# Optimization experiments

Measured on AMD Instinct MI355X. Metric: run time of the kernel, lower is better.

Reference implementation:

```python
import jax, jax.numpy as jnp
import numpy as np

N_HEAD = 8
NORM_GROUPS = 32
EPS = 1e-6


def setup_inputs() -> dict:
    key = jax.random.key(0)
    ks = jax.random.split(key, 9)
    B, C, H, W, D = 1, 256, 16, 16, 16
    COND = 512
    x = jax.random.normal(ks[0], (B, C, H, W, D), dtype=jnp.float32)
    cond = jax.random.normal(ks[1], (B, COND), dtype=jnp.float32)
    # AdaGN linear scale/shift (torch Linear: weight [C, cond_dim], bias [C])
    w_scale = jax.random.normal(ks[2], (C, COND), dtype=jnp.float32) * 0.02
    b_scale = jax.random.normal(ks[3], (C,), dtype=jnp.float32) * 0.02
    w_shift = jax.random.normal(ks[4], (C, COND), dtype=jnp.float32) * 0.02
    b_shift = jax.random.normal(ks[5], (C,), dtype=jnp.float32) * 0.02
    # 1x1x1 conv3d weights collapse to matrices: qkv [3C, C] (no bias), out [C, C] + bias
    w_qkv = jax.random.normal(ks[6], (3 * C, C), dtype=jnp.float32) * (1.0 / np.sqrt(C))
    w_out = jax.random.normal(ks[7], (C, C), dtype=jnp.float32) * (1.0 / np.sqrt(C))
    b_out = jax.random.normal(ks[8], (C,), dtype=jnp.float32) * 0.02
    return {"x": x, "cond": cond, "w_scale": w_scale, "b_scale": b_scale,
            "w_shift": w_shift, "b_shift": b_shift, "w_qkv": w_qkv,
            "w_out": w_out, "b_out": b_out}


def _ada_gn(x, cond, w_scale, b_scale, w_shift, b_shift):
    B, C, H, W, D = x.shape
    G = NORM_GROUPS
    xg = x.reshape(B, G, C // G, H, W, D)
    mean = jnp.mean(xg, axis=(2, 3, 4, 5), keepdims=True)
    var = jnp.var(xg, axis=(2, 3, 4, 5), keepdims=True)
    x_norm = ((xg - mean) * jax.lax.rsqrt(var + EPS)).reshape(B, C, H, W, D)
    scale = (cond @ w_scale.T + b_scale)[:, :, None, None, None]  # [B,C,1,1,1]
    shift = (cond @ w_shift.T + b_shift)[:, :, None, None, None]
    return x_norm * (1.0 + scale) + shift


def reference(x, cond, w_scale, b_scale, w_shift, b_shift, w_qkv, w_out, b_out):
    B, C, H, W, D = x.shape
    nh = N_HEAD
    hd = C // nh
    N = H * W * D  # flattened spatial tokens
    norm = _ada_gn(x, cond, w_scale, b_scale, w_shift, b_shift)
    # 1x1x1 conv == channel matmul
    qkv = jnp.einsum('oc,bchwd->bohwd', w_qkv, norm)        # [B,3C,H,W,D]
    qkv = qkv.reshape(B, nh, 3 * hd, N)
    q, k, v = jnp.split(qkv, 3, axis=2)                      # each [B,nh,hd,N]
    attn = jnp.einsum('bnci,bncj->bnij', q, k) / jnp.sqrt(jnp.float32(C))
    attn = jax.nn.softmax(attn, axis=-1)                     # [B,nh,N,N]
    out = jnp.einsum('bnij,bncj->bnci', attn, v)             # [B,nh,hd,N]
    out = out.reshape(B, C, H, W, D)
    out = jnp.einsum('oc,bchwd->bohwd', w_out, out) + b_out[None, :, None, None, None]
    return out + x
```

## Files before the change

kernel.cpp:

```cpp
#include <hip/hip_runtime.h>
#include <math.h>

#define CCH 256
#define NN  4096
#define NHEAD 8
#define CONDD 512

typedef __attribute__((ext_vector_type(8))) short short8;
typedef __attribute__((ext_vector_type(4))) float f32x4;
typedef __attribute__((ext_vector_type(16))) float f32x16;

static __device__ __forceinline__ short f2bf(float f) {
    union { float f; uint32_t u; } v; v.f = f;
    uint32_t r = v.u + 0x7fffu + ((v.u >> 16) & 1u);
    return (short)(r >> 16);
}

static __device__ __forceinline__ uint32_t cvt_pk_bf16(float a, float b) {
    uint32_t r;
    asm("v_cvt_pk_bf16_f32 %0, %1, %2" : "=v"(r) : "v"(a), "v"(b));
    return r;
}

__global__ __launch_bounds__(256) void front_fused(const float* __restrict__ x,
                                                   const float* __restrict__ cond,
                                                   const float* __restrict__ w_scale,
                                                   const float* __restrict__ b_scale,
                                                   const float* __restrict__ w_shift,
                                                   const float* __restrict__ b_shift,
                                                   const float* __restrict__ wq,
                                                   const float* __restrict__ wo,
                                                   float* __restrict__ partial,
                                                   float* __restrict__ scale,
                                                   float* __restrict__ shift,
                                                   short* __restrict__ wqb,
                                                   short* __restrict__ wob) {
    __shared__ float rs[4], rss[4];
    int bb = blockIdx.x;
    int t = threadIdx.x;
    if (bb < 256) {
        const float4* p = (const float4*)(x + bb * 4096);
        float s = 0.f, ss = 0.f;
        for (int k = t; k < 1024; k += 256) {
            float4 v = p[k];
            s += v.x + v.y + v.z + v.w;
            ss += v.x * v.x + v.y * v.y + v.z * v.z + v.w * v.w;
        }
        #pragma unroll
        for (int off = 32; off; off >>= 1) { s += __shfl_xor(s, off); ss += __shfl_xor(ss, off); }
        int wid = t >> 6;
        if ((t & 63) == 0) { rs[wid] = s; rss[wid] = ss; }
        __syncthreads();
        if (t == 0) {
            partial[2 * bb] = rs[0] + rs[1] + rs[2] + rs[3];
            partial[2 * bb + 1] = rss[0] + rss[1] + rss[2] + rss[3];
        }
    } else if (bb < 1280) {
        int idx = (bb - 256) * 256 + t;
        if (idx < 196608) wqb[idx] = f2bf(wq[idx]);
        else              wob[idx - 196608] = f2bf(wo[idx - 196608]);
    } else {
        int o = (bb - 1280) * 4 + (t >> 6);
        int lane = t & 63;
        float ds = 0.f, dh = 0.f;
        for (int k = lane; k < CONDD; k += 64) {
            float cv = cond[k];
            ds += cv * w_scale[o * CONDD + k];
            dh += cv * w_shift[o * CONDD + k];
        }
        #pragma unroll
        for (int off = 32; off; off >>= 1) { ds += __shfl_xor(ds, off); dh += __shfl_xor(dh, off); }
        if (lane == 0) { scale[o] = ds + b_scale[o]; shift[o] = dh + b_shift[o]; }
    }
}

__global__ __launch_bounds__(256) void normalize_t(const float* __restrict__ x,
                                                   const float* __restrict__ partial,
                                                   const float* __restrict__ scale,
                                                   const float* __restrict__ shift,
                                                   short* __restrict__ norm_t) {
    __shared__ float gm[8], gr[8];
    __shared__ float Aa[64], Bb[64];
    __shared__ short tile[32 * 66];
    int i0 = blockIdx.x * 32;
    int c0 = blockIdx.y * 64;
    int g0 = c0 >> 3;
    int t = threadIdx.x;
    if (t < 8) {
        float s = 0.f, ss = 0.f;
        #pragma unroll
        for (int ch = 0; ch < 8; ++ch) {
            s += partial[((g0 + t) * 8 + ch) * 2];
            ss += partial[((g0 + t) * 8 + ch) * 2 + 1];
        }
        float mean = s * (1.0f / 32768.0f);
        float var = ss * (1.0f / 32768.0f) - mean * mean;
        gm[t] = mean;
        gr[t] = rsqrtf(var + 1e-6f);
    }
    __syncthreads();
    if (t < 64) {
        int c = c0 + t;
        float a = gr[t >> 3] * (1.0f + scale[c]);
        Aa[t] = a;
        Bb[t] = shift[c] - gm[t >> 3] * a;
    }
    __syncthreads();
    #pragma unroll
    for (int e0 = 0; e0 < 8; ++e0) {
        int e = e0 * 256 + t;
        int cl = e >> 5, il = e & 31;
        float v = x[(c0 + cl) * NN + i0 + il];
        tile[il * 66 + cl] = f2bf(v * Aa[cl] + Bb[cl]);
    }
    __syncthreads();
    #pragma unroll
    for (int e0 = 0; e0 < 4; ++e0) {
        int e = e0 * 256 + t;
        int il = e >> 5, cd = e & 31;
        uint32_t d = *(const uint32_t*)&tile[il * 66 + 2 * cd];
        *(uint32_t*)&norm_t[(i0 + il) * 256 + c0 + 2 * cd] = d;
    }
}

__global__ __launch_bounds__(256) void qkv_gemm(const short* __restrict__ wqb,
                                                const short* __restrict__ norm_t,
                                                short* __restrict__ qtb, short* __restrict__ ktb,
                                                short* __restrict__ vcb) {
    int t = threadIdx.x;
    int w = t >> 6, lane = t & 63, li = lane & 15, lg = lane >> 4;
    int o0 = blockIdx.x * 32;
    int i0 = blockIdx.y * 64 + w * 16;
    f32x4 acc[2] = {{0,0,0,0},{0,0,0,0}};
    const short* bbase = norm_t + (i0 + li) * 256 + 8 * lg;
    const short* abase = wqb + (o0 + li) * 256 + 8 * lg;
    #pragma unroll
    for (int ks = 0; ks < 8; ++ks) {
        short8 bfrag = *(const short8*)(bbase + ks * 32);
        #pragma unroll
        for (int f = 0; f < 2; ++f) {
            short8 afrag = *(const short8*)(abase + f * 16 * 256 + ks * 32);
            acc[f] = __builtin_amdgcn_mfma_f32_16x16x32_bf16(afrag, bfrag, acc[f], 0, 0, 0);
        }
    }
    int i = i0 + li;
    #pragma unroll
    for (int f = 0; f < 2; ++f) {
        #pragma unroll
        for (int r = 0; r < 4; ++r) {
            int o = o0 + 16 * f + 4 * lg + r;
            float v = acc[f][r];
            int h = o / 96;
            int rr = o - h * 96;
            int cc = rr & 31;
            int kind = rr >> 5;
            if (kind == 0)      qtb[(h * NN + i) * 32 + cc] = f2bf(v * (0.0625f * 1.44269504f));
            else if (kind == 1) ktb[(h * NN + i) * 32 + cc] = f2bf(v);
            else                vcb[(h * 32 + cc) * NN + i] = f2bf(v);
        }
    }
}

__global__ __launch_bounds__(256, 4) void attention_mfma(const short* __restrict__ qtb,
                                                         const short* __restrict__ ktb,
                                                         const short* __restrict__ vcb,
                                                         short* __restrict__ attnT) {
    __shared__ float lds_acc[4][32][32];
    __shared__ float lds_lsum[4][32];

    int bid = blockIdx.x;
    int h = bid & 7;
    int i_base = (bid >> 3) * 32;
    int t = threadIdx.x;
    int w = t >> 6, lane = t & 63, l31 = lane & 31, hi = lane >> 5;

    const short* qrow = qtb + (h * NN + i_base + l31) * 32;
    short8 qf0 = *(const short8*)(qrow + 8 * hi);
    short8 qf1 = *(const short8*)(qrow + 16 + 8 * hi);

    const short* kbase = ktb + (h * NN + l31) * 32 + 8 * hi;
    const short* vrow  = vcb + (h * 32 + l31) * NN + 8 * hi;

    f32x16 acc = {0,0,0,0,0,0,0,0,0,0,0,0,0,0,0,0};
    const f32x16 zero16 = {0,0,0,0,0,0,0,0,0,0,0,0,0,0,0,0};
    float lsum = 0.f;

    int jstart = w * 1024;
    int jend = jstart + 1024;

    short8 kf0 = *(const short8*)(kbase + jstart * 32);
    short8 kf1 = *(const short8*)(kbase + jstart * 32 + 16);
    short8 kf2 = *(const short8*)(kbase + (jstart + 32) * 32);
    short8 kf3 = *(const short8*)(kbase + (jstart + 32) * 32 + 16);

    #pragma unroll 1
    for (int j = jstart; j < jend; j += 64) {
        short8 vf0 = *(const short8*)(vrow + j);
        short8 vf1 = *(const short8*)(vrow + j + 16);
        short8 vf2 = *(const short8*)(vrow + j + 32);
        short8 vf3 = *(const short8*)(vrow + j + 48);

        __builtin_amdgcn_s_setprio(1);
        f32x16 sa = __builtin_amdgcn_mfma_f32_32x32x16_bf16(kf0, qf0, zero16, 0, 0, 0);
        sa = __builtin_amdgcn_mfma_f32_32x32x16_bf16(kf1, qf1, sa, 0, 0, 0);
        f32x16 sb = __builtin_amdgcn_mfma_f32_32x32x16_bf16(kf2, qf0, zero16, 0, 0, 0);
        sb = __builtin_amdgcn_mfma_f32_32x32x16_bf16(kf3, qf1, sb, 0, 0, 0);
        __builtin_amdgcn_s_setprio(0);

        if (j + 64 < jend) {
            kf0 = *(const short8*)(kbase + (j + 64) * 32);
            kf1 = *(const short8*)(kbase + (j + 64) * 32 + 16);
            kf2 = *(const short8*)(kbase + (j + 96) * 32);
            kf3 = *(const short8*)(kbase + (j + 96) * 32 + 16);
        }

        float pa[16], pb[16];
        #pragma unroll
        for (int r = 0; r < 16; ++r) pa[r] = __builtin_amdgcn_exp2f(sa[r]);
        #pragma unroll
        for (int r = 0; r < 16; ++r) pb[r] = __builtin_amdgcn_exp2f(sb[r]);

        float u0 = 0.f, u1 = 0.f, u2 = 0.f, u3 = 0.f;
        #pragma unroll
        for (int r = 0; r < 4; ++r) {
            u0 += pa[r] + pa[4 + r];
            u1 += pa[8 + r] + pa[12 + r];
            u2 += pb[r] + pb[4 + r];
            u3 += pb[8 + r] + pb[12 + r];
        }
        lsum += (u0 + u1) + (u2 + u3);

        auto A1 = __builtin_amdgcn_permlane32_swap(cvt_pk_bf16(pa[0], pa[1]),   cvt_pk_bf16(pa[4], pa[5]),   false, false);
        auto A2 = __builtin_amdgcn_permlane32_swap(cvt_pk_bf16(pa[2], pa[3]),   cvt_pk_bf16(pa[6], pa[7]),   false, false);
        auto A3 = __builtin_amdgcn_permlane32_swap(cvt_pk_bf16(pa[8], pa[9]),   cvt_pk_bf16(pa[12], pa[13]), false, false);
        auto A4 = __builtin_amdgcn_permlane32_swap(cvt_pk_bf16(pa[10], pa[11]), cvt_pk_bf16(pa[14], pa[15]), false, false);
        auto B1 = __builtin_amdgcn_permlane32_swap(cvt_pk_bf16(pb[0], pb[1]),   cvt_pk_bf16(pb[4], pb[5]),   false, false);
        auto B2 = __builtin_amdgcn_permlane32_swap(cvt_pk_bf16(pb[2], pb[3]),   cvt_pk_bf16(pb[6], pb[7]),   false, false);
        auto B3 = __builtin_amdgcn_permlane32_swap(cvt_pk_bf16(pb[8], pb[9]),   cvt_pk_bf16(pb[12], pb[13]), false, false);
        auto B4 = __builtin_amdgcn_permlane32_swap(cvt_pk_bf16(pb[10], pb[11]), cvt_pk_bf16(pb[14], pb[15]), false, false);

        union PF { uint32_t u[4]; short8 s8; };
        PF fa1, fa2, fb1, fb2;
        fa1.u[0] = A1[0]; fa1.u[1] = A2[0]; fa1.u[2] = A1[1]; fa1.u[3] = A2[1];
        fa2.u[0] = A3[0]; fa2.u[1] = A4[0]; fa2.u[2] = A3[1]; fa2.u[3] = A4[1];
        fb1.u[0] = B1[0]; fb1.u[1] = B2[0]; fb1.u[2] = B1[1]; fb1.u[3] = B2[1];
        fb2.u[0] = B3[0]; fb2.u[1] = B4[0]; fb2.u[2] = B3[1]; fb2.u[3] = B4[1];

        __builtin_amdgcn_s_setprio(1);
        acc = __builtin_amdgcn_mfma_f32_32x32x16_bf16(vf0, fa1.s8, acc, 0, 0, 0);
        acc = __builtin_amdgcn_mfma_f32_32x32x16_bf16(vf1, fa2.s8, acc, 0, 0, 0);
        acc = __builtin_amdgcn_mfma_f32_32x32x16_bf16(vf2, fb1.s8, acc, 0, 0, 0);
        acc = __builtin_amdgcn_mfma_f32_32x32x16_bf16(vf3, fb2.s8, acc, 0, 0, 0);
        __builtin_amdgcn_s_setprio(0);
    }

    lsum += __shfl_xor(lsum, 32);

    #pragma unroll
    for (int r = 0; r < 16; ++r) {
        int c = (r & 3) + 8 * (r >> 2) + 4 * hi;
        lds_acc[w][c][l31] = acc[r];
    }
    if (hi == 0) lds_lsum[w][l31] = lsum;
    __syncthreads();

    int q = t & 31, c0 = (t >> 5) * 4;
    float s0 = 0.f, s1 = 0.f, s2 = 0.f, s3 = 0.f, ls = 0.f;
    #pragma unroll
    for (int ww = 0; ww < 4; ++ww) {
        s0 += lds_acc[ww][c0 + 0][q];
        s1 += lds_acc[ww][c0 + 1][q];
        s2 += lds_acc[ww][c0 + 2][q];
        s3 += lds_acc[ww][c0 + 3][q];
        ls += lds_lsum[ww][q];
    }
    float inv = 1.0f / ls;
    uint2 uu;
    uu.x = cvt_pk_bf16(s0 * inv, s1 * inv);
    uu.y = cvt_pk_bf16(s2 * inv, s3 * inv);
    *(uint2*)&attnT[(i_base + q) * 256 + h * 32 + c0] = uu;
}

__global__ __launch_bounds__(256) void proj_gemm(const short* __restrict__ wob,
                                                 const short* __restrict__ attnT,
                                                 const float* __restrict__ b_out,
                                                 const float* __restrict__ x,
                                                 float* __restrict__ out) {
    int t = threadIdx.x;
    int w = t >> 6, lane = t & 63, li = lane & 15, lg = lane >> 4;
    int o0 = blockIdx.x * 32;
    int i0 = blockIdx.y * 64 + w * 16;
    f32x4 acc[2] = {{0,0,0,0},{0,0,0,0}};
    const short* bbase = attnT + (i0 + li) * 256 + 8 * lg;
    const short* abase = wob + (o0 + li) * 256 + 8 * lg;
    #pragma unroll
    for (int ks = 0; ks < 8; ++ks) {
        short8 bfrag = *(const short8*)(bbase + ks * 32);
        #pragma unroll
        for (int f = 0; f < 2; ++f) {
            short8 afrag = *(const short8*)(abase + f * 16 * 256 + ks * 32);
            acc[f] = __builtin_amdgcn_mfma_f32_16x16x32_bf16(afrag, bfrag, acc[f], 0, 0, 0);
        }
    }
    int i = i0 + li;
    #pragma unroll
    for (int f = 0; f < 2; ++f) {
        #pragma unroll
        for (int r = 0; r < 4; ++r) {
            int o = o0 + 16 * f + 4 * lg + r;
            out[o * NN + i] = acc[f][r] + b_out[o] + x[o * NN + i];
        }
    }
}

extern "C" void kernel_launch(void* const* d_in, const int* in_sizes, int n_in,
                              void* d_out, int out_size, void* d_ws, size_t ws_size,
                              hipStream_t stream) {
    const float* x       = (const float*)d_in[0];
    const float* cond    = (const float*)d_in[1];
    const float* w_scale = (const float*)d_in[2];
    const float* b_scale = (const float*)d_in[3];
    const float* w_shift = (const float*)d_in[4];
    const float* b_shift = (const float*)d_in[5];
    const float* w_qkv   = (const float*)d_in[6];
    const float* w_out   = (const float*)d_in[7];
    const float* b_out   = (const float*)d_in[8];
    float* out = (float*)d_out;

    float* ws = (float*)d_ws;
    float* scale   = ws;
    float* shift   = ws + 256;
    float* partial = ws + 512;
    short* norm_t = (short*)(ws + 1024);
    short* qtb = norm_t + 1048576;
    short* ktb = qtb + 1048576;
    short* vcb = ktb + 1048576;
    short* attnT = vcb + 1048576;
    short* wqb = attnT + 1048576;
    short* wob = wqb + 768 * 256;

    front_fused<<<1344, 256, 0, stream>>>(x, cond, w_scale, b_scale, w_shift, b_shift,
                                          w_qkv, w_out, partial, scale, shift, wqb, wob);
    normalize_t<<<dim3(128, 4), 256, 0, stream>>>(x, partial, scale, shift, norm_t);
    qkv_gemm<<<dim3(24, 64), 256, 0, stream>>>(wqb, norm_t, qtb, ktb, vcb);
    attention_mfma<<<1024, 256, 0, stream>>>(qtb, ktb, vcb, attnT);
    proj_gemm<<<dim3(8, 64), 256, 0, stream>>>(wob, attnT, b_out, x, out);
}
```

Before: 86.28 us.

## Software-pipeline attention loop so QK of next tile overlaps softmax-PV of current

Restructures the attention inner loop into 32-key tiles with a two-stage software pipeline. The QK MFMA for the next tile is issued before the exp/convert/PV work of the previous tile, and K/V loads are prefetched one tile ahead. This aims to hide MFMA latency and memory latency behind the VALU softmax work. It raises register pressure by keeping two score tiles live, which may affect occupancy at launch_bounds(256,4).

```diff
diff --git a/kernel.cpp b/kernel.cpp
--- a/kernel.cpp
+++ b/kernel.cpp
@@ -161,6 +161,39 @@
     }
 }
 
+union PF { uint32_t u[4]; short8 s8; };
+
+static __device__ __forceinline__ f32x16 qk_tile(short8 k0, short8 k1, short8 qf0, short8 qf1) {
+    const f32x16 z = {0,0,0,0,0,0,0,0,0,0,0,0,0,0,0,0};
+    __builtin_amdgcn_s_setprio(1);
+    f32x16 s = __builtin_amdgcn_mfma_f32_32x32x16_bf16(k0, qf0, z, 0, 0, 0);
+    s = __builtin_amdgcn_mfma_f32_32x32x16_bf16(k1, qf1, s, 0, 0, 0);
+    __builtin_amdgcn_s_setprio(0);
+    return s;
+}
+
+static __device__ __forceinline__ void pv_tile(f32x16 s, short8 v0, short8 v1,
+                                               f32x16& acc, float& lsum) {
+    float p[16];
+    #pragma unroll
+    for (int r = 0; r < 16; ++r) p[r] = __builtin_amdgcn_exp2f(s[r]);
+    float u0 = 0.f, u1 = 0.f;
+    #pragma unroll
+    for (int r = 0; r < 4; ++r) { u0 += p[r] + p[4 + r]; u1 += p[8 + r] + p[12 + r]; }
+    lsum += u0 + u1;
+    auto A1 = __builtin_amdgcn_permlane32_swap(cvt_pk_bf16(p[0], p[1]),   cvt_pk_bf16(p[4], p[5]),   false, false);
+    auto A2 = __builtin_amdgcn_permlane32_swap(cvt_pk_bf16(p[2], p[3]),   cvt_pk_bf16(p[6], p[7]),   false, false);
+    auto A3 = __builtin_amdgcn_permlane32_swap(cvt_pk_bf16(p[8], p[9]),   cvt_pk_bf16(p[12], p[13]), false, false);
+    auto A4 = __builtin_amdgcn_permlane32_swap(cvt_pk_bf16(p[10], p[11]), cvt_pk_bf16(p[14], p[15]), false, false);
+    PF f1, f2;
+    f1.u[0] = A1[0]; f1.u[1] = A2[0]; f1.u[2] = A1[1]; f1.u[3] = A2[1];
+    f2.u[0] = A3[0]; f2.u[1] = A4[0]; f2.u[2] = A3[1]; f2.u[3] = A4[1];
+    __builtin_amdgcn_s_setprio(1);
+    acc = __builtin_amdgcn_mfma_f32_32x32x16_bf16(v0, f1.s8, acc, 0, 0, 0);
+    acc = __builtin_amdgcn_mfma_f32_32x32x16_bf16(v1, f2.s8, acc, 0, 0, 0);
+    __builtin_amdgcn_s_setprio(0);
+}
+
 __global__ __launch_bounds__(256, 4) void attention_mfma(const short* __restrict__ qtb,
                                                          const short* __restrict__ ktb,
                                                          const short* __restrict__ vcb,
@@ -182,77 +215,34 @@
     const short* vrow  = vcb + (h * 32 + l31) * NN + 8 * hi;
 
     f32x16 acc = {0,0,0,0,0,0,0,0,0,0,0,0,0,0,0,0};
-    const f32x16 zero16 = {0,0,0,0,0,0,0,0,0,0,0,0,0,0,0,0};
     float lsum = 0.f;
 
     int jstart = w * 1024;
-    int jend = jstart + 1024;
-
-    short8 kf0 = *(const short8*)(kbase + jstart * 32);
-    short8 kf1 = *(const short8*)(kbase + jstart * 32 + 16);
-    short8 kf2 = *(const short8*)(kbase + (jstart + 32) * 32);
-    short8 kf3 = *(const short8*)(kbase + (jstart + 32) * 32 + 16);
+    const short* kp = kbase + jstart * 32;
+    const short* vp = vrow + jstart;
+
+    short8 k0 = *(const short8*)kp, k1 = *(const short8*)(kp + 16);
+    short8 v0 = *(const short8*)vp, v1 = *(const short8*)(vp + 16);
+    f32x16 sA = qk_tile(k0, k1, qf0, qf1);
+    kp += 1024; k0 = *(const short8*)kp; k1 = *(const short8*)(kp + 16);
+    f32x16 sB;
 
     #pragma unroll 1
-    for (int j = jstart; j < jend; j += 64) {
-        short8 vf0 = *(const short8*)(vrow + j);
-        short8 vf1 = *(const short8*)(vrow + j + 16);
-        short8 vf2 = *(const short8*)(vrow + j + 32);
-        short8 vf3 = *(const short8*)(vrow + j + 48);
-
-        __builtin_amdgcn_s_setprio(1);
-        f32x16 sa = __builtin_amdgcn_mfma_f32_32x32x16_bf16(kf0, qf0, zero16, 0, 0, 0);
-        sa = __builtin_amdgcn_mfma_f32_32x32x16_bf16(kf1, qf1, sa, 0, 0, 0);
-        f32x16 sb = __builtin_amdgcn_mfma_f32_32x32x16_bf16(kf2, qf0, zero16, 0, 0, 0);
-        sb = __builtin_amdgcn_mfma_f32_32x32x16_bf16(kf3, qf1, sb, 0, 0, 0);
-        __builtin_amdgcn_s_setprio(0);
-
-        if (j + 64 < jend) {
-            kf0 = *(const short8*)(kbase + (j + 64) * 32);
-            kf1 = *(const short8*)(kbase + (j + 64) * 32 + 16);
-            kf2 = *(const short8*)(kbase + (j + 96) * 32);
-            kf3 = *(const short8*)(kbase + (j + 96) * 32 + 16);
-        }
-
-        float pa[16], pb[16];
-        #pragma unroll
-        for (int r = 0; r < 16; ++r) pa[r] = __builtin_amdgcn_exp2f(sa[r]);
-        #pragma unroll
-        for (int r = 0; r < 16; ++r) pb[r] = __builtin_amdgcn_exp2f(sb[r]);
-
-        float u0 = 0.f, u1 = 0.f, u2 = 0.f, u3 = 0.f;
-        #pragma unroll
-        for (int r = 0; r < 4; ++r) {
-            u0 += pa[r] + pa[4 + r];
-            u1 += pa[8 + r] + pa[12 + r];
-            u2 += pb[r] + pb[4 + r];
-            u3 += pb[8 + r] + pb[12 + r];
-        }
-        lsum += (u0 + u1) + (u2 + u3);
-
-        auto A1 = __builtin_amdgcn_permlane32_swap(cvt_pk_bf16(pa[0], pa[1]),   cvt_pk_bf16(pa[4], pa[5]),   false, false);
-        auto A2 = __builtin_amdgcn_permlane32_swap(cvt_pk_bf16(pa[2], pa[3]),   cvt_pk_bf16(pa[6], pa[7]),   false, false);
-        auto A3 = __builtin_amdgcn_permlane32_swap(cvt_pk_bf16(pa[8], pa[9]),   cvt_pk_bf16(pa[12], pa[13]), false, false);
-        auto A4 = __builtin_amdgcn_permlane32_swap(cvt_pk_bf16(pa[10], pa[11]), cvt_pk_bf16(pa[14], pa[15]), false, false);
-        auto B1 = __builtin_amdgcn_permlane32_swap(cvt_pk_bf16(pb[0], pb[1]),   cvt_pk_bf16(pb[4], pb[5]),   false, false);
-        auto B2 = __builtin_amdgcn_permlane32_swap(cvt_pk_bf16(pb[2], pb[3]),   cvt_pk_bf16(pb[6], pb[7]),   false, false);
-        auto B3 = __builtin_amdgcn_permlane32_swap(cvt_pk_bf16(pb[8], pb[9]),   cvt_pk_bf16(pb[12], pb[13]), false, false);
-        auto B4 = __builtin_amdgcn_permlane32_swap(cvt_pk_bf16(pb[10], pb[11]), cvt_pk_bf16(pb[14], pb[15]), false, false);
-
-        union PF { uint32_t u[4]; short8 s8; };
-        PF fa1, fa2, fb1, fb2;
-        fa1.u[0] = A1[0]; fa1.u[1] = A2[0]; fa1.u[2] = A1[1]; fa1.u[3] = A2[1];
-        fa2.u[0] = A3[0]; fa2.u[1] = A4[0]; fa2.u[2] = A3[1]; fa2.u[3] = A4[1];
-        fb1.u[0] = B1[0]; fb1.u[1] = B2[0]; fb1.u[2] = B1[1]; fb1.u[3] = B2[1];
-        fb2.u[0] = B3[0]; fb2.u[1] = B4[0]; fb2.u[2] = B3[1]; fb2.u[3] = B4[1];
-
-        __builtin_amdgcn_s_setprio(1);
-        acc = __builtin_amdgcn_mfma_f32_32x32x16_bf16(vf0, fa1.s8, acc, 0, 0, 0);
-        acc = __builtin_amdgcn_mfma_f32_32x32x16_bf16(vf1, fa2.s8, acc, 0, 0, 0);
-        acc = __builtin_amdgcn_mfma_f32_32x32x16_bf16(vf2, fb1.s8, acc, 0, 0, 0);
-        acc = __builtin_amdgcn_mfma_f32_32x32x16_bf16(vf3, fb2.s8, acc, 0, 0, 0);
-        __builtin_amdgcn_s_setprio(0);
-    }
+    for (int p = 0; p < 15; ++p) {
+        sB = qk_tile(k0, k1, qf0, qf1);
+        kp += 1024; k0 = *(const short8*)kp; k1 = *(const short8*)(kp + 16);
+        pv_tile(sA, v0, v1, acc, lsum);
+        vp += 32; v0 = *(const short8*)vp; v1 = *(const short8*)(vp + 16);
+
+        sA = qk_tile(k0, k1, qf0, qf1);
+        kp += 1024; k0 = *(const short8*)kp; k1 = *(const short8*)(kp + 16);
+        pv_tile(sB, v0, v1, acc, lsum);
+        vp += 32; v0 = *(const short8*)vp; v1 = *(const short8*)(vp + 16);
+    }
+    sB = qk_tile(k0, k1, qf0, qf1);
+    pv_tile(sA, v0, v1, acc, lsum);
+    vp += 32; v0 = *(const short8*)vp; v1 = *(const short8*)(vp + 16);
+    pv_tile(sB, v0, v1, acc, lsum);
 
     lsum += __shfl_xor(lsum, 32);
 
```

Result: no change. 86.56 us (+0.3%).
